# Performance work log

Measured on AMD Instinct MI355X. Metric: run time of the kernel, lower is better.

The kernel has to match this reference:

```python
import jax, jax.numpy as jnp
import numpy as np

N_USERS = 50000
N_ENT = 100000
N_EDGES = 2_000_000
N_INTER = 1_000_000
CHANNEL = 64
N_HEADS = 2
D_K = CHANNEL // N_HEADS
N_HOPS = 2
N_REL = 10  # relation_emb has N_REL-1 rows


def setup_inputs() -> dict:
    key = jax.random.key(0)
    ks = jax.random.split(key, 8)
    user_emb = jax.random.normal(ks[0], (N_USERS, CHANNEL), jnp.float32) * 0.1
    entity_emb = jax.random.normal(ks[1], (N_ENT, CHANNEL), jnp.float32) * 0.1
    relation_emb = jax.random.normal(ks[2], (N_REL - 1, CHANNEL), jnp.float32) * 0.1
    W_Q = jax.random.normal(ks[3], (CHANNEL, CHANNEL), jnp.float32) * (1.0 / np.sqrt(CHANNEL))
    edge_index = jax.random.randint(ks[4], (2, N_EDGES), 0, N_ENT)
    edge_type = jax.random.randint(ks[5], (N_EDGES,), 1, N_REL)  # in [1, N_REL-1]
    inter_edge = jnp.stack([
        jax.random.randint(ks[6], (N_INTER,), 0, N_USERS),
        jax.random.randint(ks[7], (N_INTER,), 0, N_ENT),
    ])
    inter_edge_w = jnp.full((N_INTER,), 1.0 / 20.0, jnp.float32)
    return {
        "user_emb": user_emb,
        "entity_emb": entity_emb,
        "relation_emb": relation_emb,
        "W_Q": W_Q,
        "inter_edge_w": inter_edge_w,
        "edge_index": edge_index,
        "edge_type": edge_type,
        "inter_edge": inter_edge,
    }


def _l2norm(x):
    # F.normalize(dim=-1) with eps=1e-12
    n = jnp.linalg.norm(x, axis=-1, keepdims=True)
    return x / jnp.maximum(n, 1e-12)


def _scatter_softmax(logits, seg, num_segments):
    # per-segment (over leading axis) numerically-stable softmax; logits [E, H]
    m = jax.ops.segment_max(logits, seg, num_segments=num_segments)
    e = jnp.exp(logits - m[seg])
    s = jax.ops.segment_sum(e, seg, num_segments=num_segments)
    return e / s[seg]


def reference(user_emb, entity_emb, relation_emb, W_Q, inter_edge_w,
              edge_index, edge_type, inter_edge):
    head, tail = edge_index[0], edge_index[1]
    u_idx, i_idx = inter_edge[0], inter_edge[1]
    rel = relation_emb[edge_type - 1]  # [E, C]
    inv_sqrt_dk = 1.0 / np.sqrt(D_K)

    entity_res, user_res = entity_emb, user_emb
    for _ in range(N_HOPS):
        h_emb = entity_emb[head]                       # [E, C]
        t_emb = entity_emb[tail]                       # [E, C]
        q = (h_emb @ W_Q).reshape(-1, N_HEADS, D_K)    # [E, H, Dk]
        k = (t_emb @ W_Q).reshape(-1, N_HEADS, D_K) * rel.reshape(-1, N_HEADS, D_K)
        score = (q * k).sum(-1) * inv_sqrt_dk          # [E, H]
        attn = _scatter_softmax(score, head, N_ENT)    # [E, H]
        value = (t_emb * rel).reshape(-1, N_HEADS, D_K)
        agg = (value * attn[..., None]).reshape(-1, CHANNEL)
        entity_agg = jax.ops.segment_sum(agg, head, num_segments=N_ENT)
        item_agg = inter_edge_w[:, None] * entity_emb[i_idx]
        user_agg = jax.ops.segment_sum(item_agg, u_idx, num_segments=N_USERS)
        # mess_dropout disabled (eval mode)
        entity_emb = _l2norm(entity_agg)
        user_emb = _l2norm(user_agg)
        entity_res = entity_res + entity_emb
        user_res = user_res + user_emb
    return entity_res, user_res
```

## Files before the change

### kernel.cpp

```cpp
#include <hip/hip_runtime.h>

#define NU     50000
#define NEN    100000
#define NEDGE  2000000
#define NINTER 1000000
#define CH     64
#define NRELM1 9
#define CAPE   64
#define CAPU   64

typedef _Float16 hv2 __attribute__((ext_vector_type(2)));
typedef _Float16 h8  __attribute__((ext_vector_type(8)));
typedef float    f32x4 __attribute__((ext_vector_type(4)));
union P4 { float4 f; hv2 h[4]; };

__global__ __launch_bounds__(256) void k_setup(
    const float* __restrict__ ue, const float* __restrict__ ee,
    const float* __restrict__ re, const float* __restrict__ wq,
    const float* __restrict__ iw, const int* __restrict__ eidx,
    const int* __restrict__ etype, const int* __restrict__ ii,
    _Float16* __restrict__ Eh, float* __restrict__ Eres, float* __restrict__ Ures,
    _Float16* __restrict__ Relh, _Float16* __restrict__ Wt,
    int* __restrict__ cntE, int* __restrict__ cntU,
    int* __restrict__ csrE, unsigned long long* __restrict__ csrU2)
{
    int i = blockIdx.x * 256 + threadIdx.x;
    if (i < NEN * CH) {
        float f = ee[i];
        Eh[i] = (_Float16)f;
        Eres[i] = f;
    }
    if (i < NU * CH)     Ures[i] = ue[i];
    if (i < NRELM1 * CH) Relh[i] = (_Float16)re[i];
    if (i < CH * CH)     Wt[(i & 63) * 64 + (i >> 6)] = (_Float16)wq[i];
    if (i < NEDGE) {
        int head = eidx[i], tail = eidx[NEDGE + i], rt = etype[i] - 1;
        int pos = atomicAdd(&cntE[head], 1);
        if (pos < CAPE)
            __hip_atomic_store(&csrE[head * CAPE + pos], tail | (rt << 17),
                               __ATOMIC_RELAXED, __HIP_MEMORY_SCOPE_AGENT);
    }
    if (i < NINTER) {
        int u = ii[i], ent = ii[NINTER + i];
        int pos = atomicAdd(&cntU[u], 1);
        unsigned long long rec = (unsigned long long)(unsigned)ent
                               | ((unsigned long long)__float_as_uint(iw[i]) << 32);
        if (pos < CAPU)
            __hip_atomic_store(&csrU2[(size_t)u * CAPU + pos], rec,
                               __ATOMIC_RELAXED, __HIP_MEMORY_SCOPE_AGENT);
    }
}

__global__ __launch_bounds__(256) void k_gemm(
    const _Float16* __restrict__ Eh, const _Float16* __restrict__ Wt,
    _Float16* __restrict__ Qh)
{
    int w = threadIdx.x >> 6, lane = threadIdx.x & 63;
    int r0 = blockIdx.x * 64 + w * 16;
    if (r0 >= NEN) return;
    int lr = lane & 15, lg = lane >> 4;
    const _Float16* arow = Eh + (size_t)(r0 + lr) * 64 + lg * 8;
    h8 a0 = *(const h8*)(arow);
    h8 a1 = *(const h8*)(arow + 32);
#pragma unroll
    for (int ct = 0; ct < 4; ++ct) {
        const _Float16* brow = Wt + (ct * 16 + lr) * 64 + lg * 8;
        h8 b0 = *(const h8*)(brow);
        h8 b1 = *(const h8*)(brow + 32);
        f32x4 c = {0.f, 0.f, 0.f, 0.f};
        c = __builtin_amdgcn_mfma_f32_16x16x32_f16(a0, b0, c, 0, 0, 0);
        c = __builtin_amdgcn_mfma_f32_16x16x32_f16(a1, b1, c, 0, 0, 0);
#pragma unroll
        for (int r = 0; r < 4; ++r)
            Qh[(size_t)(r0 + lg * 4 + r) * 64 + ct * 16 + lr] = (_Float16)c[r];
    }
}

__global__ __launch_bounds__(256) void k_fused(
    const int* __restrict__ cntE, const int* __restrict__ csrE,
    const _Float16* __restrict__ Qh, const _Float16* __restrict__ Eh,
    const _Float16* __restrict__ Relh,
    _Float16* __restrict__ Ehn, float* __restrict__ Eres,
    const int* __restrict__ cntU, const unsigned long long* __restrict__ csrU2,
    float* __restrict__ Ures)
{
    int wid  = blockIdx.x * 4 + (threadIdx.x >> 6);
    int lane = threadIdx.x & 63;
    int s = lane >> 3, l = lane & 7;
    int c8 = l * 8;

    if (wid < NEN) {
        int row = wid;
        int cnt = cntE[row]; if (cnt > CAPE) cnt = CAPE;
        int beg = row * CAPE, end = beg + cnt;
        P4 q; q.f = *(const float4*)(Qh + (size_t)row * 64 + c8);
        float acc[8] = {0.f,0.f,0.f,0.f,0.f,0.f,0.f,0.f};
        float den = 0.f;
        int a0 = beg + s;
        int pA = (a0 < end) ? csrE[a0] : 0;
        int pB = (a0 + 8 < end) ? csrE[a0 + 8] : 0;
        P4 ktA, teA, rlA;
        {
            int tail = pA & 0x1FFFF, rt = pA >> 17;
            ktA.f = *(const float4*)(Qh   + (size_t)tail * 64 + c8);
            teA.f = *(const float4*)(Eh   + (size_t)tail * 64 + c8);
            rlA.f = *(const float4*)(Relh + rt * 64 + c8);
        }
        int nit = (cnt + 7) >> 3;
        for (int it = 0; it < nit; ++it) {
            P4 ktB, teB, rlB;
            int tailB = pB & 0x1FFFF, rtB = pB >> 17;
            ktB.f = *(const float4*)(Qh   + (size_t)tailB * 64 + c8);
            teB.f = *(const float4*)(Eh   + (size_t)tailB * 64 + c8);
            rlB.f = *(const float4*)(Relh + rtB * 64 + c8);
            int a2 = beg + (it + 2) * 8 + s;
            int pN = (a2 < end) ? csrE[a2] : 0;
            bool act = (beg + it * 8 + s) < end;
            float sc = 0.f;
#pragma unroll
            for (int i = 0; i < 4; ++i) {
                hv2 km = ktA.h[i] * rlA.h[i];
                sc = __builtin_amdgcn_fdot2(q.h[i], km, sc, false);
            }
            sc += __shfl_xor(sc, 1);
            sc += __shfl_xor(sc, 2);
            float ex = act ? __expf(sc * 0.17677669529663687f) : 0.f;
            den += ex;
#pragma unroll
            for (int i = 0; i < 4; ++i) {
                hv2 vm = teA.h[i] * rlA.h[i];
                acc[2*i]   += ex * (float)vm.x;
                acc[2*i+1] += ex * (float)vm.y;
            }
            ktA = ktB; teA = teB; rlA = rlB; pB = pN;
        }
#pragma unroll
        for (int k = 0; k < 8; ++k) {
            acc[k] += __shfl_xor(acc[k], 8);
            acc[k] += __shfl_xor(acc[k], 16);
            acc[k] += __shfl_xor(acc[k], 32);
        }
        den += __shfl_xor(den, 8); den += __shfl_xor(den, 16); den += __shfl_xor(den, 32);
        float invd = (den > 0.f) ? 1.f / den : 0.f;
        float ss = 0.f;
#pragma unroll
        for (int k = 0; k < 8; ++k) { acc[k] *= invd; ss += acc[k] * acc[k]; }
        ss += __shfl_xor(ss, 1); ss += __shfl_xor(ss, 2); ss += __shfl_xor(ss, 4);
        float inv = 1.f / fmaxf(sqrtf(ss), 1e-12f);
#pragma unroll
        for (int k = 0; k < 8; ++k) acc[k] *= inv;
        if (s == 0) {
            P4 o;
#pragma unroll
            for (int i = 0; i < 4; ++i) { o.h[i].x = (_Float16)acc[2*i]; o.h[i].y = (_Float16)acc[2*i+1]; }
            *(float4*)(Ehn + (size_t)row * 64 + c8) = o.f;
            float4 r0 = *(const float4*)(Eres + (size_t)row * 64 + c8);
            float4 r1 = *(const float4*)(Eres + (size_t)row * 64 + c8 + 4);
            r0.x += acc[0]; r0.y += acc[1]; r0.z += acc[2]; r0.w += acc[3];
            r1.x += acc[4]; r1.y += acc[5]; r1.z += acc[6]; r1.w += acc[7];
            *(float4*)(Eres + (size_t)row * 64 + c8)     = r0;
            *(float4*)(Eres + (size_t)row * 64 + c8 + 4) = r1;
        }
    } else {
        int row = wid - NEN;
        int cnt = cntU[row]; if (cnt > CAPU) cnt = CAPU;
        int beg = row * CAPU, end = beg + cnt;
        float acc[8] = {0.f,0.f,0.f,0.f,0.f,0.f,0.f,0.f};
        int a0 = beg + s;
        unsigned long long recA = (a0 < end) ? csrU2[a0] : 0ull;
        unsigned long long recB = (a0 + 8 < end) ? csrU2[a0 + 8] : 0ull;
        P4 teA; teA.f = *(const float4*)(Eh + (size_t)(unsigned)recA * 64 + c8);
        int nit = (cnt + 7) >> 3;
        for (int it = 0; it < nit; ++it) {
            P4 teB; teB.f = *(const float4*)(Eh + (size_t)(unsigned)recB * 64 + c8);
            int a2 = beg + (it + 2) * 8 + s;
            unsigned long long recN = (a2 < end) ? csrU2[a2] : 0ull;
            float wgt = __uint_as_float((unsigned)(recA >> 32));
#pragma unroll
            for (int i = 0; i < 4; ++i) {
                acc[2*i]   += wgt * (float)teA.h[i].x;
                acc[2*i+1] += wgt * (float)teA.h[i].y;
            }
            teA = teB; recA = recB; recB = recN;
        }
#pragma unroll
        for (int k = 0; k < 8; ++k) {
            acc[k] += __shfl_xor(acc[k], 8);
            acc[k] += __shfl_xor(acc[k], 16);
            acc[k] += __shfl_xor(acc[k], 32);
        }
        float ss = 0.f;
#pragma unroll
        for (int k = 0; k < 8; ++k) ss += acc[k] * acc[k];
        ss += __shfl_xor(ss, 1); ss += __shfl_xor(ss, 2); ss += __shfl_xor(ss, 4);
        float inv = 1.f / fmaxf(sqrtf(ss), 1e-12f);
        if (s == 0) {
            float4 r0 = *(const float4*)(Ures + (size_t)row * 64 + c8);
            float4 r1 = *(const float4*)(Ures + (size_t)row * 64 + c8 + 4);
            r0.x += acc[0] * inv; r0.y += acc[1] * inv; r0.z += acc[2] * inv; r0.w += acc[3] * inv;
            r1.x += acc[4] * inv; r1.y += acc[5] * inv; r1.z += acc[6] * inv; r1.w += acc[7] * inv;
            *(float4*)(Ures + (size_t)row * 64 + c8)     = r0;
            *(float4*)(Ures + (size_t)row * 64 + c8 + 4) = r1;
        }
    }
}

extern "C" void kernel_launch(void* const* d_in, const int* in_sizes, int n_in,
                              void* d_out, int out_size, void* d_ws, size_t ws_size,
                              hipStream_t stream)
{
    const float* ue = (const float*)d_in[0];
    const float* ee = (const float*)d_in[1];
    const float* re = (const float*)d_in[2];
    const float* wq = (const float*)d_in[3];
    const float* iw = (const float*)d_in[4];
    const int* eidx  = (const int*)d_in[5];
    const int* etype = (const int*)d_in[6];
    const int* ii    = (const int*)d_in[7];

    float* Eres = (float*)d_out;
    float* Ures = Eres + (size_t)NEN * CH;

    _Float16* Relh = (_Float16*)d_ws;
    _Float16* Wt   = Relh + 1024;
    _Float16* Qh   = Wt + 4096;
    _Float16* EhA  = Qh  + (size_t)NEN * CH;
    _Float16* EhB  = EhA + (size_t)NEN * CH;
    int* cntE      = (int*)(EhB + (size_t)NEN * CH);
    int* cntU      = cntE + NEN;
    int* csrE      = cntU + NU;
    unsigned long long* csrU2 = (unsigned long long*)(csrE + (size_t)NEN * CAPE);

    hipMemsetAsync(cntE, 0, (size_t)(NEN + NU) * sizeof(int), stream);
    k_setup<<<(NEN * CH) / 256, 256, 0, stream>>>(ue, ee, re, wq, iw, eidx, etype, ii,
                                                  EhA, Eres, Ures, Relh, Wt,
                                                  cntE, cntU, csrE, csrU2);

    _Float16* Ehc = EhA;
    _Float16* Ehn = EhB;
    for (int hop = 0; hop < 2; ++hop) {
        k_gemm <<<(NEN + 63) / 64, 256, 0, stream>>>(Ehc, Wt, Qh);
        k_fused<<<(NEN + NU) / 4, 256, 0, stream>>>(cntE, csrE, Qh, Ehc, Relh,
                                                    Ehn, Eres, cntU, csrU2, Ures);
        _Float16* tmp = Ehc; Ehc = Ehn; Ehn = tmp;
    }
}
```

Before: 508.9 us.

## Build adjacency via two-pass shared-memory binning instead of global atomics

Replaces the single setup kernel, which used per-node global atomicAdd and scattered stores to build capped adjacency lists, with a two-pass bucketing scheme. The first pass histograms edges into 256-node bins in shared memory and reserves bin ranges with one global atomic per bin. The second pass places records into per-node slots using shared-memory atomics, and it also writes the clamped counts so the memset on the count arrays is no longer needed. Vectorized embedding conversion and copies run inside the same launch. The change adds a kernel launch and relies on fixed bin capacities, reusing the Qh and EhB workspaces as staging buffers.

```diff
diff --git a/kernel.cpp b/kernel.cpp
--- a/kernel.cpp
+++ b/kernel.cpp
@@ -9,45 +9,155 @@
 #define CAPE   64
 #define CAPU   64
 
+#define BINSH   8
+#define NBINE   ((NEN + 255) >> BINSH)
+#define NBINU   ((NU  + 255) >> BINSH)
+#define CAPBE   6144
+#define CAPBU   6144
+#define CHUNK   8192
+#define NBE_BLK ((NEDGE  + CHUNK - 1) / CHUNK)
+#define NBU_BLK ((NINTER + CHUNK - 1) / CHUNK)
+#define NSTR_E  ((NEN * CH) / 2048)
+#define NSTR_U  ((NU * CH + 2047) / 2048)
+
 typedef _Float16 hv2 __attribute__((ext_vector_type(2)));
 typedef _Float16 h8  __attribute__((ext_vector_type(8)));
 typedef float    f32x4 __attribute__((ext_vector_type(4)));
 union P4 { float4 f; hv2 h[4]; };
 
-__global__ __launch_bounds__(256) void k_setup(
+__global__ __launch_bounds__(256) void k_bin(
     const float* __restrict__ ue, const float* __restrict__ ee,
     const float* __restrict__ re, const float* __restrict__ wq,
     const float* __restrict__ iw, const int* __restrict__ eidx,
     const int* __restrict__ etype, const int* __restrict__ ii,
     _Float16* __restrict__ Eh, float* __restrict__ Eres, float* __restrict__ Ures,
     _Float16* __restrict__ Relh, _Float16* __restrict__ Wt,
-    int* __restrict__ cntE, int* __restrict__ cntU,
-    int* __restrict__ csrE, unsigned long long* __restrict__ csrU2)
-{
-    int i = blockIdx.x * 256 + threadIdx.x;
-    if (i < NEN * CH) {
-        float f = ee[i];
-        Eh[i] = (_Float16)f;
-        Eres[i] = f;
-    }
-    if (i < NU * CH)     Ures[i] = ue[i];
-    if (i < NRELM1 * CH) Relh[i] = (_Float16)re[i];
-    if (i < CH * CH)     Wt[(i & 63) * 64 + (i >> 6)] = (_Float16)wq[i];
-    if (i < NEDGE) {
-        int head = eidx[i], tail = eidx[NEDGE + i], rt = etype[i] - 1;
-        int pos = atomicAdd(&cntE[head], 1);
-        if (pos < CAPE)
-            __hip_atomic_store(&csrE[head * CAPE + pos], tail | (rt << 17),
-                               __ATOMIC_RELAXED, __HIP_MEMORY_SCOPE_AGENT);
-    }
-    if (i < NINTER) {
-        int u = ii[i], ent = ii[NINTER + i];
-        int pos = atomicAdd(&cntU[u], 1);
-        unsigned long long rec = (unsigned long long)(unsigned)ent
-                               | ((unsigned long long)__float_as_uint(iw[i]) << 32);
-        if (pos < CAPU)
-            __hip_atomic_store(&csrU2[(size_t)u * CAPU + pos], rec,
-                               __ATOMIC_RELAXED, __HIP_MEMORY_SCOPE_AGENT);
+    int* __restrict__ binCurE, int* __restrict__ binCurU,
+    int* __restrict__ binBufE, unsigned long long* __restrict__ binBufU)
+{
+    __shared__ int hist[NBINE];
+    __shared__ int gbase[NBINE];
+    int b = blockIdx.x, tid = threadIdx.x;
+
+    if (b < NBE_BLK) {
+        for (int i = tid; i < NBINE; i += 256) hist[i] = 0;
+        __syncthreads();
+        int base = b * CHUNK;
+        int n = NEDGE - base; if (n > CHUNK) n = CHUNK;
+        for (int i = tid; i < n; i += 256)
+            atomicAdd(&hist[eidx[base + i] >> BINSH], 1);
+        __syncthreads();
+        for (int i = tid; i < NBINE; i += 256) {
+            int c = hist[i];
+            gbase[i] = c ? atomicAdd(&binCurE[i], c) : 0;
+            hist[i] = 0;
+        }
+        __syncthreads();
+        for (int i = tid; i < n; i += 256) {
+            int h  = eidx[base + i];
+            int t  = eidx[NEDGE + base + i];
+            int rt = etype[base + i] - 1;
+            int bin = h >> BINSH;
+            int pos = atomicAdd(&hist[bin], 1);
+            int g = gbase[bin] + pos;
+            if (g < CAPBE)
+                __hip_atomic_store(&binBufE[bin * CAPBE + g],
+                                   (h & 255) | ((t | (rt << 17)) << 8),
+                                   __ATOMIC_RELAXED, __HIP_MEMORY_SCOPE_AGENT);
+        }
+    } else if (b < NBE_BLK + NBU_BLK) {
+        for (int i = tid; i < NBINU; i += 256) hist[i] = 0;
+        __syncthreads();
+        int base = (b - NBE_BLK) * CHUNK;
+        int n = NINTER - base; if (n > CHUNK) n = CHUNK;
+        for (int i = tid; i < n; i += 256)
+            atomicAdd(&hist[ii[base + i] >> BINSH], 1);
+        __syncthreads();
+        for (int i = tid; i < NBINU; i += 256) {
+            int c = hist[i];
+            gbase[i] = c ? atomicAdd(&binCurU[i], c) : 0;
+            hist[i] = 0;
+        }
+        __syncthreads();
+        for (int i = tid; i < n; i += 256) {
+            int u = ii[base + i];
+            int e = ii[NINTER + base + i];
+            unsigned w = __float_as_uint(iw[base + i]);
+            int bin = u >> BINSH;
+            int pos = atomicAdd(&hist[bin], 1);
+            int g = gbase[bin] + pos;
+            if (g < CAPBU)
+                __hip_atomic_store(&binBufU[bin * CAPBU + g],
+                                   (unsigned long long)((u & 255) | (e << 8))
+                                 | ((unsigned long long)w << 32),
+                                   __ATOMIC_RELAXED, __HIP_MEMORY_SCOPE_AGENT);
+        }
+    } else {
+        int sb = b - (NBE_BLK + NBU_BLK);
+        if (sb < NSTR_E) {
+            int i0 = sb * 2048 + tid * 8;
+            float4 a = *(const float4*)(ee + i0);
+            float4 c = *(const float4*)(ee + i0 + 4);
+            *(float4*)(Eres + i0)     = a;
+            *(float4*)(Eres + i0 + 4) = c;
+            P4 o;
+            o.h[0].x = (_Float16)a.x; o.h[0].y = (_Float16)a.y;
+            o.h[1].x = (_Float16)a.z; o.h[1].y = (_Float16)a.w;
+            o.h[2].x = (_Float16)c.x; o.h[2].y = (_Float16)c.y;
+            o.h[3].x = (_Float16)c.z; o.h[3].y = (_Float16)c.w;
+            *(float4*)(Eh + i0) = o.f;
+        } else if (sb < NSTR_E + NSTR_U) {
+            int i0 = (sb - NSTR_E) * 2048 + tid * 8;
+            if (i0 < NU * CH) {
+                *(float4*)(Ures + i0)     = *(const float4*)(ue + i0);
+                *(float4*)(Ures + i0 + 4) = *(const float4*)(ue + i0 + 4);
+            }
+        } else {
+            for (int i = tid; i < NRELM1 * CH; i += 256)
+                Relh[i] = (_Float16)re[i];
+            for (int i = tid; i < CH * CH; i += 256)
+                Wt[(i & 63) * 64 + (i >> 6)] = (_Float16)wq[i];
+        }
+    }
+}
+
+__global__ __launch_bounds__(256) void k_place(
+    const int* __restrict__ binCurE, const int* __restrict__ binBufE,
+    const int* __restrict__ binCurU, const unsigned long long* __restrict__ binBufU,
+    int* __restrict__ cntE, int* __restrict__ csrE,
+    int* __restrict__ cntU, unsigned long long* __restrict__ csrU2)
+{
+    __shared__ int cnt[256];
+    int b = blockIdx.x, tid = threadIdx.x;
+    cnt[tid] = 0;
+    __syncthreads();
+    if (b < NBINE) {
+        int n = binCurE[b]; if (n > CAPBE) n = CAPBE;
+        const int* buf = binBufE + b * CAPBE;
+        for (int i = tid; i < n; i += 256) {
+            int rec = buf[i];
+            int nl = rec & 255;
+            int pos = atomicAdd(&cnt[nl], 1);
+            if (pos < CAPE) csrE[((b << BINSH) + nl) * CAPE + pos] = rec >> 8;
+        }
+        __syncthreads();
+        int node = (b << BINSH) + tid;
+        if (node < NEN) { int c = cnt[tid]; cntE[node] = c > CAPE ? CAPE : c; }
+    } else {
+        int ub = b - NBINE;
+        int n = binCurU[ub]; if (n > CAPBU) n = CAPBU;
+        const unsigned long long* buf = binBufU + ub * CAPBU;
+        for (int i = tid; i < n; i += 256) {
+            unsigned long long rec = buf[i];
+            int nl = (int)rec & 255;
+            int pos = atomicAdd(&cnt[nl], 1);
+            if (pos < CAPU)
+                csrU2[((ub << BINSH) + nl) * CAPU + pos] =
+                    ((rec & 0xFFFFFFFFull) >> 8) | (rec & 0xFFFFFFFF00000000ull);
+        }
+        __syncthreads();
+        int node = (ub << BINSH) + tid;
+        if (node < NU) { int c = cnt[tid]; cntU[node] = c > CAPU ? CAPU : c; }
     }
 }
 
@@ -91,7 +201,7 @@
 
     if (wid < NEN) {
         int row = wid;
-        int cnt = cntE[row]; if (cnt > CAPE) cnt = CAPE;
+        int cnt = cntE[row];
         int beg = row * CAPE, end = beg + cnt;
         P4 q; q.f = *(const float4*)(Qh + (size_t)row * 64 + c8);
         float acc[8] = {0.f,0.f,0.f,0.f,0.f,0.f,0.f,0.f};
@@ -163,7 +273,7 @@
         }
     } else {
         int row = wid - NEN;
-        int cnt = cntU[row]; if (cnt > CAPU) cnt = CAPU;
+        int cnt = cntU[row];
         int beg = row * CAPU, end = beg + cnt;
         float acc[8] = {0.f,0.f,0.f,0.f,0.f,0.f,0.f,0.f};
         int a0 = beg + s;
@@ -230,11 +340,17 @@
     int* cntU      = cntE + NEN;
     int* csrE      = cntU + NU;
     unsigned long long* csrU2 = (unsigned long long*)(csrE + (size_t)NEN * CAPE);
-
-    hipMemsetAsync(cntE, 0, (size_t)(NEN + NU) * sizeof(int), stream);
-    k_setup<<<(NEN * CH) / 256, 256, 0, stream>>>(ue, ee, re, wq, iw, eidx, etype, ii,
-                                                  EhA, Eres, Ures, Relh, Wt,
-                                                  cntE, cntU, csrE, csrU2);
+    int* binCurE   = (int*)(csrU2 + (size_t)NU * CAPU);
+    int* binCurU   = binCurE + NBINE;
+    int* binBufE   = (int*)Qh;
+    unsigned long long* binBufU = (unsigned long long*)EhB;
+
+    hipMemsetAsync(binCurE, 0, (NBINE + NBINU) * sizeof(int), stream);
+    k_bin<<<NBE_BLK + NBU_BLK + NSTR_E + NSTR_U + 1, 256, 0, stream>>>(
+        ue, ee, re, wq, iw, eidx, etype, ii,
+        EhA, Eres, Ures, Relh, Wt, binCurE, binCurU, binBufE, binBufU);
+    k_place<<<NBINE + NBINU, 256, 0, stream>>>(binCurE, binBufE, binCurU, binBufU,
+                                               cntE, csrE, cntU, csrU2);
 
     _Float16* Ehc = EhA;
     _Float16* Ehn = EhB;
```

New measurement: 471.8 us. 1.08x faster.
